# Kernel tuning notes

Measured on AMD Instinct MI355X. Metric: run time of the kernel, lower is better.

The kernel has to match this reference:

```python
import jax, jax.numpy as jnp
import numpy as np

B, S, D, M = 2, 4096, 128, 64

def _linear_init(key, shape, fan_in):
    bound = 1.0 / np.sqrt(fan_in)
    return jax.random.uniform(key, shape, jnp.float32, -bound, bound)

def setup_inputs() -> dict:
    key = jax.random.key(0)
    ks = jax.random.split(key, 18)
    x = jax.random.normal(ks[0], (B, S, D), jnp.float32)
    context = jax.random.normal(ks[1], (B, S, D), jnp.float32)
    # per-mechanism params (torch Linear semantics: y = x @ W.T + b)
    Wt = _linear_init(ks[2], (M, D, D), D)   # transform weight, laid out [m, in, out]
    bt = _linear_init(ks[3], (M, D), D)
    char = jax.random.normal(ks[4], (M, D), jnp.float32)  # characteristics [1,1,d] per mech
    Wg = _linear_init(ks[5], (M, D), D)      # timing_gate weight (out=1)
    bg = _linear_init(ks[6], (M,), D)
    Wv = _linear_init(ks[7], (M, D), D)      # victory_detector weight (out=1)
    bv = _linear_init(ks[8], (M,), D)
    O = jax.random.normal(ks[9], (M, M), jnp.float32) * 0.02  # overcoming matrix
    # selector: Linear(2D,2D) -> GELU -> Linear(2D,M)
    W1 = _linear_init(ks[10], (2 * D, 2 * D), 2 * D)
    b1 = _linear_init(ks[11], (2 * D,), 2 * D)
    W2 = _linear_init(ks[12], (2 * D, M), 2 * D)
    b2 = _linear_init(ks[13], (M,), 2 * D)
    # integrate: Linear(2D, D)
    Wi = _linear_init(ks[14], (2 * D, D), 2 * D)
    bi = _linear_init(ks[15], (D,), 2 * D)
    return {"x": x, "context": context, "Wt": Wt, "bt": bt, "char": char,
            "Wg": Wg, "bg": bg, "Wv": Wv, "bv": bv, "O": O,
            "W1": W1, "b1": b1, "W2": W2, "b2": b2, "Wi": Wi, "bi": bi}

def reference(x, context, Wt, bt, char, Wg, bg, Wv, bv, O, W1, b1, W2, b2, Wi, bi):
    # selection scores over mechanisms
    sel_in = jnp.concatenate([x, context], axis=-1)          # [b,s,2d]
    h = jax.nn.gelu(sel_in @ W1 + b1, approximate=False)
    selection_scores = jax.nn.softmax(h @ W2 + b2, axis=-1)  # [b,s,m]
    # all 64 mechanism nodes as one batched GEMM
    transformed = jnp.einsum('bsd,mde->bsme', x, Wt) + bt + char   # [b,s,m,d]
    timing = jax.nn.sigmoid(jnp.einsum('bsd,md->bsm', x, Wg) + bg)  # [b,s,m]
    victory = jax.nn.sigmoid(jnp.einsum('bsme,me->bsm', transformed, Wv) + bv)
    outputs = transformed * timing[..., None]                # [b,s,m,d]
    # strategic overcoming modulation: gate = 1 + tanh(scores @ O)
    gates = 1.0 + jnp.tanh(selection_scores @ O)             # [b,s,m]
    selected = jnp.einsum('bsme,bsm->bse', outputs, gates * selection_scores)
    victory_potential = jnp.sum(victory * selection_scores, axis=-1)  # [b,s]
    integrated = jnp.concatenate([x, selected], axis=-1) @ Wi + bi    # [b,s,d]
    return integrated, victory_potential
```

## Files before the change

### kernel.cpp

```cpp
#include <hip/hip_runtime.h>
#include <hip/hip_bf16.h>


typedef __bf16 bf16_t;
typedef __bf16 bf16x8 __attribute__((ext_vector_type(8)));
typedef float  f32x4  __attribute__((ext_vector_type(4)));

#define WS_WTT      0u
#define WS_W1T      2097152u
#define WS_W2T      2228224u
#define WS_OT       2260992u
#define WS_WG       2269184u
#define WS_U        2285568u
#define WS_CVEC     2301952u
#define WS_BCT      2302208u
#define WS_WIT      2318592u

#define VP_OFF 1048576

__device__ __forceinline__ f32x4 mfma16(bf16x8 a, bf16x8 b, f32x4 c) {
  return __builtin_amdgcn_mfma_f32_16x16x32_bf16(a, b, c, 0, 0, 0);
}

__device__ __forceinline__ float gelu_exact(float v) {
  return 0.5f * v * (1.0f + erff(v * 0.70710678118654752f));
}
__device__ __forceinline__ float sigmoidf_(float v) {
  return 1.0f / (1.0f + __expf(-v));
}

__device__ __forceinline__ bf16x8 cvt8(float4 v0, float4 v1) {
  bf16x8 a;
  a[0] = (bf16_t)v0.x; a[1] = (bf16_t)v0.y; a[2] = (bf16_t)v0.z; a[3] = (bf16_t)v0.w;
  a[4] = (bf16_t)v1.x; a[5] = (bf16_t)v1.y; a[6] = (bf16_t)v1.z; a[7] = (bf16_t)v1.w;
  return a;
}

__global__ __launch_bounds__(256) void kprep(
    const float* __restrict__ Wt, const float* __restrict__ bt,
    const float* __restrict__ ch, const float* __restrict__ Wg,
    const float* __restrict__ Wv, const float* __restrict__ bv,
    const float* __restrict__ O, const float* __restrict__ W1,
    const float* __restrict__ W2, const float* __restrict__ Wi,
    char* __restrict__ ws)
{
  const int bid = blockIdx.x, tid = threadIdx.x;
  if (bid < 128) {
    const int m = bid >> 1, half = bid & 1;
    const float* wtm = Wt + m * 16384;
    bf16_t* wtt = (bf16_t*)(ws + WS_WTT) + m * 16384;
    const int ks = half * 2 + (tid >> 7), e = tid & 127;
    bf16_t tmp[32];
    #pragma unroll
    for (int dd = 0; dd < 32; ++dd)
      tmp[dd] = (bf16_t)wtm[(ks * 32 + dd) * 128 + e];
    bf16_t* dst = wtt + ks * 4096 + e * 32;
    #pragma unroll
    for (int g = 0; g < 4; ++g)
      *(bf16x8*)(dst + g * 8) = *(const bf16x8*)(tmp + g * 8);
    if (half == 0) {
      if (tid < 128) {
        const float* wvm = Wv + m * 128;
        float s = 0.f;
        for (int e2 = 0; e2 < 128; ++e2) s += wtm[tid * 128 + e2] * wvm[e2];
        ((bf16_t*)(ws + WS_U))[m * 128 + tid] = (bf16_t)s;
      } else if (tid == 128) {
        const float* wvm = Wv + m * 128;
        float s = bv[m];
        for (int e2 = 0; e2 < 128; ++e2) s += (bt[m * 128 + e2] + ch[m * 128 + e2]) * wvm[e2];
        ((float*)(ws + WS_CVEC))[m] = s;
      }
    }
  } else if (bid < 144) {
    int base = (bid - 128) * 256 + tid;
    int k = base >> 4, c0 = (base & 15) * 16;
    bf16_t* o = (bf16_t*)(ws + WS_W1T);
    #pragma unroll
    for (int j = 0; j < 16; ++j) o[(c0 + j) * 256 + k] = (bf16_t)W1[k * 256 + c0 + j];
  } else if (bid < 146) {
    int base = (bid - 144) * 256 + tid;
    int k = base >> 1, c0 = (base & 1) * 32;
    bf16_t* o = (bf16_t*)(ws + WS_W2T);
    #pragma unroll
    for (int j = 0; j < 32; ++j) o[(c0 + j) * 256 + k] = (bf16_t)W2[k * 64 + c0 + j];
  } else if (bid == 146) {
    int k = tid >> 2, c0 = (tid & 3) * 16;
    bf16_t* o = (bf16_t*)(ws + WS_OT);
    #pragma unroll
    for (int j = 0; j < 16; ++j) o[(c0 + j) * 64 + k] = (bf16_t)O[k * 64 + c0 + j];
  } else if (bid == 147) {
    bf16_t* o = (bf16_t*)(ws + WS_WG);
    #pragma unroll
    for (int j = 0; j < 32; ++j) o[tid * 32 + j] = (bf16_t)Wg[tid * 32 + j];
  } else if (bid == 148) {
    bf16_t* o = (bf16_t*)(ws + WS_BCT);
    #pragma unroll
    for (int i = 0; i < 4; ++i) {
      int task = tid + i * 256;
      int m = task >> 4, e0 = (task & 15) * 8;
      #pragma unroll
      for (int j = 0; j < 8; ++j)
        o[(e0 + j) * 64 + m] = (bf16_t)(bt[m * 128 + e0 + j] + ch[m * 128 + e0 + j]);
    }
  } else {
    int base = (bid - 149) * 256 + tid;
    int k = base >> 2, c0 = (base & 3) * 32;
    bf16_t* o = (bf16_t*)(ws + WS_WIT);
    #pragma unroll
    for (int j = 0; j < 32; ++j) o[(c0 + j) * 256 + k] = (bf16_t)Wi[k * 128 + c0 + j];
  }
}

__device__ __forceinline__ void loadF(bf16x8 (&F)[4], const char* bbase, int m) {
  const char* p = bbase + m * 32768;
  F[0] = *(const bf16x8*)(p);
  F[1] = *(const bf16x8*)(p + 8192);
  F[2] = *(const bf16x8*)(p + 16384);
  F[3] = *(const bf16x8*)(p + 24576);
}

template<int J>
__device__ __forceinline__ void computeT(const bf16x8 (&F)[4], const f32x4 (&wc)[16],
                                         const bf16x8 (&aSel)[4][8], f32x4 (&acc)[4]) {
  #pragma unroll
  for (int rg = 0; rg < 4; ++rg) {
    f32x4 y = {0.f, 0.f, 0.f, 0.f};
    #pragma unroll
    for (int ks = 0; ks < 4; ++ks) y = mfma16(aSel[rg][ks], F[ks], y);
    #pragma unroll
    for (int jj = 0; jj < 4; ++jj)
      acc[rg][jj] += wc[rg * 4 + jj][J] * y[jj];
  }
}

__global__ __launch_bounds__(256, 1) void kfused(
    const float* __restrict__ x, const float* __restrict__ ctx,
    const float* __restrict__ b1, const float* __restrict__ b2,
    const float* __restrict__ bg, const float* __restrict__ bi,
    char* __restrict__ ws, float* __restrict__ out)
{
  __shared__ char sm[92160];
  bf16_t* hL      = (bf16_t*)sm;
  float*  scoresL = (float*)(sm + 32768);
  float*  wL      = (float*)(sm + 49152);
  bf16_t* scbL    = (bf16_t*)(sm + 66560);
  bf16_t* wbL     = (bf16_t*)(sm + 74752);
  bf16_t* selL    = (bf16_t*)(sm + 82944);
  float*  vpL     = (float*)(sm + 91136);

  const int tid = threadIdx.x;
  const int lane = tid & 63, wid = tid >> 6;
  const int tb = (blockIdx.x >> 1) * 64;
  const int eh = blockIdx.x & 1;
  const int lr = lane & 15;
  const int lg = lane >> 4;
  const int lk = lg * 8;
  const int lj4 = lg * 4;

  const bf16_t* W1t = (const bf16_t*)(ws + WS_W1T);
  const bf16_t* W2t = (const bf16_t*)(ws + WS_W2T);
  const bf16_t* Ot  = (const bf16_t*)(ws + WS_OT);
  const bf16_t* Wgb = (const bf16_t*)(ws + WS_WG);
  const bf16_t* Ub  = (const bf16_t*)(ws + WS_U);
  const float*  cv  = (const float*)(ws + WS_CVEC);
  const bf16_t* bct = (const bf16_t*)(ws + WS_BCT);
  const bf16_t* Wit = (const bf16_t*)(ws + WS_WIT);
  const char*  wttc = (const char*)(ws + WS_WTT);

  bf16x8 aSel[4][8];
  #pragma unroll
  for (int rg = 0; rg < 4; ++rg) {
    int t = tb + rg * 16 + lr;
    #pragma unroll
    for (int ks = 0; ks < 8; ++ks) {
      const float* src = (ks < 4) ? (x + t * 128 + ks * 32 + lk)
                                  : (ctx + t * 128 + (ks - 4) * 32 + lk);
      aSel[rg][ks] = cvt8(*(const float4*)src, *(const float4*)(src + 4));
    }
  }

  #pragma unroll
  for (int cg = 0; cg < 4; ++cg) {
    int c = wid * 64 + cg * 16 + lr;
    f32x4 a[4] = {{0,0,0,0},{0,0,0,0},{0,0,0,0},{0,0,0,0}};
    #pragma unroll
    for (int ks = 0; ks < 8; ++ks) {
      bf16x8 b = *(const bf16x8*)(W1t + c * 256 + ks * 32 + lk);
      #pragma unroll
      for (int rg = 0; rg < 4; ++rg) a[rg] = mfma16(aSel[rg][ks], b, a[rg]);
    }
    float bb = b1[c];
    #pragma unroll
    for (int rg = 0; rg < 4; ++rg)
      #pragma unroll
      for (int j = 0; j < 4; ++j) {
        int r = rg * 16 + lj4 + j;
        float v = gelu_exact(a[rg][j] + bb);
        *(bf16_t*)((char*)hL + ((r * 512 + c * 2) ^ ((r & 7) << 4))) = (bf16_t)v;
      }
  }
  __syncthreads();

  {
    int c = wid * 16 + lr;
    f32x4 l[4] = {{0,0,0,0},{0,0,0,0},{0,0,0,0},{0,0,0,0}};
    #pragma unroll
    for (int ks = 0; ks < 8; ++ks) {
      int k0 = ks * 32 + lk;
      bf16x8 b = *(const bf16x8*)(W2t + c * 256 + k0);
      #pragma unroll
      for (int rg = 0; rg < 4; ++rg) {
        int r = rg * 16 + lr;
        bf16x8 a = *(const bf16x8*)((char*)hL + ((r * 512 + k0 * 2) ^ ((r & 7) << 4)));
        l[rg] = mfma16(a, b, l[rg]);
      }
    }
    float bb = b2[c];
    #pragma unroll
    for (int rg = 0; rg < 4; ++rg)
      #pragma unroll
      for (int j = 0; j < 4; ++j)
        scoresL[(rg * 16 + lj4 + j) * 64 + c] = l[rg][j] + bb;
  }
  __syncthreads();

  {
    int row = tid >> 2, i = tid & 3;
    float v[16];
    #pragma unroll
    for (int j = 0; j < 16; ++j) v[j] = scoresL[row * 64 + i * 16 + j];
    float mx = v[0];
    #pragma unroll
    for (int j = 1; j < 16; ++j) mx = fmaxf(mx, v[j]);
    mx = fmaxf(mx, __shfl_xor(mx, 1));
    mx = fmaxf(mx, __shfl_xor(mx, 2));
    float sum = 0.f;
    #pragma unroll
    for (int j = 0; j < 16; ++j) { v[j] = __expf(v[j] - mx); sum += v[j]; }
    sum += __shfl_xor(sum, 1);
    sum += __shfl_xor(sum, 2);
    float inv = 1.0f / sum;
    #pragma unroll
    for (int j = 0; j < 16; ++j) {
      float s = v[j] * inv;
      int cc = i * 16 + j;
      scoresL[row * 64 + cc] = s;
      *(bf16_t*)((char*)scbL + ((row * 128 + cc * 2) ^ ((row & 7) << 4))) = (bf16_t)s;
    }
  }
  __syncthreads();

  {
    const int c = wid * 16 + lr;
    f32x4 g[4] = {{0,0,0,0},{0,0,0,0},{0,0,0,0},{0,0,0,0}};
    #pragma unroll
    for (int ks = 0; ks < 2; ++ks) {
      int k0 = ks * 32 + lk;
      bf16x8 b = *(const bf16x8*)(Ot + c * 64 + k0);
      #pragma unroll
      for (int rg = 0; rg < 4; ++rg) {
        int r = rg * 16 + lr;
        bf16x8 a = *(const bf16x8*)((char*)scbL + ((r * 128 + k0 * 2) ^ ((r & 7) << 4)));
        g[rg] = mfma16(a, b, g[rg]);
      }
    }
    f32x4 t[4] = {{0,0,0,0},{0,0,0,0},{0,0,0,0},{0,0,0,0}};
    f32x4 v[4] = {{0,0,0,0},{0,0,0,0},{0,0,0,0},{0,0,0,0}};
    #pragma unroll
    for (int ks = 0; ks < 4; ++ks) {
      bf16x8 bT = *(const bf16x8*)(Wgb + c * 128 + ks * 32 + lk);
      bf16x8 bV = *(const bf16x8*)(Ub  + c * 128 + ks * 32 + lk);
      #pragma unroll
      for (int rg = 0; rg < 4; ++rg) {
        t[rg] = mfma16(aSel[rg][ks], bT, t[rg]);
        v[rg] = mfma16(aSel[rg][ks], bV, v[rg]);
      }
    }
    float bgc = bg[c], cvc = cv[c];
    #pragma unroll
    for (int rg = 0; rg < 4; ++rg)
      #pragma unroll
      for (int j = 0; j < 4; ++j) {
        int r = rg * 16 + lj4 + j;
        float gate = 1.0f + tanhf(g[rg][j]);
        float tim  = sigmoidf_(t[rg][j] + bgc);
        float vic  = sigmoidf_(v[rg][j] + cvc);
        float sc   = scoresL[r * 64 + c];
        float w    = gate * sc * tim;
        wL[r * 68 + c] = w;
        *(bf16_t*)((char*)wbL + ((r * 128 + c * 2) ^ ((r & 7) << 4))) = (bf16_t)w;
        float pv = vic * sc;
        pv += __shfl_xor(pv, 1); pv += __shfl_xor(pv, 2);
        pv += __shfl_xor(pv, 4); pv += __shfl_xor(pv, 8);
        if (lr == 0) vpL[r * 4 + wid] = pv;
      }
  }
  __syncthreads();

  if (eh == 0 && tid < 64) {
    float s = vpL[tid * 4 + 0] + vpL[tid * 4 + 1] + vpL[tid * 4 + 2] + vpL[tid * 4 + 3];
    out[VP_OFF + tb + tid] = s;
  }

  const int wcol = wid * 16;
  f32x4 acc[4] = {{0,0,0,0},{0,0,0,0},{0,0,0,0},{0,0,0,0}};
  {
    int eg = eh * 64 + wcol + lr;
    #pragma unroll
    for (int ks = 0; ks < 2; ++ks) {
      int k0 = ks * 32 + lk;
      bf16x8 b = *(const bf16x8*)(bct + eg * 64 + k0);
      #pragma unroll
      for (int rg = 0; rg < 4; ++rg) {
        int r = rg * 16 + lr;
        bf16x8 a = *(const bf16x8*)((char*)wbL + ((r * 128 + k0 * 2) ^ ((r & 7) << 4)));
        acc[rg] = mfma16(a, b, acc[rg]);
      }
    }
  }

  const char* bbase = wttc + (size_t)(((eh * 64 + wcol + lr) * 32 + lg * 8) * 2);
  bf16x8 F0[4], F1[4], F2[4], F3[4];
  loadF(F0, bbase, 0);
  loadF(F1, bbase, 1);
  loadF(F2, bbase, 2);

  for (int it = 0; it < 16; ++it) {
    const int base = it * 4;
    f32x4 wc[16];
    #pragma unroll
    for (int rg = 0; rg < 4; ++rg)
      #pragma unroll
      for (int jj = 0; jj < 4; ++jj)
        wc[rg * 4 + jj] = *(const f32x4*)(&wL[(rg * 16 + lj4 + jj) * 68 + base]);
    int n4 = base + 4 > 63 ? 63 : base + 4;
    int n5 = base + 5 > 63 ? 63 : base + 5;
    int n6 = base + 6 > 63 ? 63 : base + 6;
    loadF(F3, bbase, base + 3);
    computeT<0>(F0, wc, aSel, acc);
    loadF(F0, bbase, n4);
    computeT<1>(F1, wc, aSel, acc);
    loadF(F1, bbase, n5);
    computeT<2>(F2, wc, aSel, acc);
    loadF(F2, bbase, n6);
    computeT<3>(F3, wc, aSel, acc);
  }

  #pragma unroll
  for (int rg = 0; rg < 4; ++rg)
    #pragma unroll
    for (int j = 0; j < 4; ++j) {
      int r = rg * 16 + lj4 + j;
      int cl = wcol + lr;
      *(bf16_t*)((char*)selL + ((r * 128 + cl * 2) ^ ((r & 7) << 4))) = (bf16_t)acc[rg][j];
    }
  __syncthreads();

  #pragma unroll
  for (int cg = 0; cg < 2; ++cg) {
    int c = wid * 32 + cg * 16 + lr;
    f32x4 a[4] = {{0,0,0,0},{0,0,0,0},{0,0,0,0},{0,0,0,0}};
    #pragma unroll
    for (int ks = 0; ks < 2; ++ks) {
      int k0 = ks * 32 + lk;
      bf16x8 b = *(const bf16x8*)(Wit + c * 256 + 128 + eh * 64 + k0);
      #pragma unroll
      for (int rg = 0; rg < 4; ++rg) {
        int r = rg * 16 + lr;
        bf16x8 av = *(const bf16x8*)((char*)selL + ((r * 128 + k0 * 2) ^ ((r & 7) << 4)));
        a[rg] = mfma16(av, b, a[rg]);
      }
    }
    if (eh == 0) {
      #pragma unroll
      for (int ks = 0; ks < 4; ++ks) {
        bf16x8 b = *(const bf16x8*)(Wit + c * 256 + ks * 32 + lk);
        #pragma unroll
        for (int rg = 0; rg < 4; ++rg) a[rg] = mfma16(aSel[rg][ks], b, a[rg]);
      }
    }
    float bb = (eh == 0) ? bi[c] : 0.0f;
    #pragma unroll
    for (int rg = 0; rg < 4; ++rg)
      #pragma unroll
      for (int j = 0; j < 4; ++j)
        atomicAdd(&out[(tb + rg * 16 + lj4 + j) * 128 + c], a[rg][j] + bb);
  }
}

extern "C" void kernel_launch(void* const* d_in, const int* in_sizes, int n_in,
                              void* d_out, int out_size, void* d_ws, size_t ws_size,
                              hipStream_t stream)
{
  (void)in_sizes; (void)n_in; (void)ws_size;
  const float* x   = (const float*)d_in[0];
  const float* ctx = (const float*)d_in[1];
  const float* Wt  = (const float*)d_in[2];
  const float* bt  = (const float*)d_in[3];
  const float* ch  = (const float*)d_in[4];
  const float* Wg  = (const float*)d_in[5];
  const float* bg  = (const float*)d_in[6];
  const float* Wv  = (const float*)d_in[7];
  const float* bv  = (const float*)d_in[8];
  const float* O   = (const float*)d_in[9];
  const float* W1  = (const float*)d_in[10];
  const float* b1  = (const float*)d_in[11];
  const float* W2  = (const float*)d_in[12];
  const float* b2  = (const float*)d_in[13];
  const float* Wi  = (const float*)d_in[14];
  const float* bi  = (const float*)d_in[15];
  float* out = (float*)d_out;
  char* ws = (char*)d_ws;

  hipMemsetAsync(d_out, 0, (size_t)out_size * 4, stream);
  kprep<<<153, 256, 0, stream>>>(Wt, bt, ch, Wg, Wv, bv, O, W1, W2, Wi, ws);
  kfused<<<256, 256, 0, stream>>>(x, ctx, b1, b2, bg, bi, ws, out);
}
```

Before: 146.8 us.

## Split fused kernel rows across 8 waves and parallelize U/cvec prep

The fused kernel now runs 512 threads per block. Waves are split into two row halves of 32 tokens each, which halves the per-wave register fragments and accumulators and doubles the waves available to hide latency. The softmax pass is remapped to 8 threads per row. In the prep kernel, the serial Wt·Wv reduction and the bias/char·Wv reduction move into dedicated extra blocks that use vectorized float4 loads instead of a long scalar loop in a few blocks. The trade-off is that each wave reloads the Wt B-fragments for fewer rows, which raises L2 and global traffic per useful MFMA.

```diff
diff --git a/kernel.cpp b/kernel.cpp
--- a/kernel.cpp
+++ b/kernel.cpp
@@ -58,19 +58,6 @@
     #pragma unroll
     for (int g = 0; g < 4; ++g)
       *(bf16x8*)(dst + g * 8) = *(const bf16x8*)(tmp + g * 8);
-    if (half == 0) {
-      if (tid < 128) {
-        const float* wvm = Wv + m * 128;
-        float s = 0.f;
-        for (int e2 = 0; e2 < 128; ++e2) s += wtm[tid * 128 + e2] * wvm[e2];
-        ((bf16_t*)(ws + WS_U))[m * 128 + tid] = (bf16_t)s;
-      } else if (tid == 128) {
-        const float* wvm = Wv + m * 128;
-        float s = bv[m];
-        for (int e2 = 0; e2 < 128; ++e2) s += (bt[m * 128 + e2] + ch[m * 128 + e2]) * wvm[e2];
-        ((float*)(ws + WS_CVEC))[m] = s;
-      }
-    }
   } else if (bid < 144) {
     int base = (bid - 128) * 256 + tid;
     int k = base >> 4, c0 = (base & 15) * 16;
@@ -102,12 +89,38 @@
       for (int j = 0; j < 8; ++j)
         o[(e0 + j) * 64 + m] = (bf16_t)(bt[m * 128 + e0 + j] + ch[m * 128 + e0 + j]);
     }
-  } else {
+  } else if (bid < 153) {
     int base = (bid - 149) * 256 + tid;
     int k = base >> 2, c0 = (base & 3) * 32;
     bf16_t* o = (bf16_t*)(ws + WS_WIT);
     #pragma unroll
     for (int j = 0; j < 32; ++j) o[(c0 + j) * 256 + k] = (bf16_t)Wi[k * 128 + c0 + j];
+  } else if (bid < 185) {
+    int task = (bid - 153) * 256 + tid;
+    int m = task >> 7, d = task & 127;
+    const float4* wp = (const float4*)(Wt + m * 16384 + d * 128);
+    const float4* vp = (const float4*)(Wv + m * 128);
+    float s = 0.f;
+    #pragma unroll
+    for (int i = 0; i < 32; ++i) {
+      float4 a = wp[i], b = vp[i];
+      s += a.x * b.x + a.y * b.y + a.z * b.z + a.w * b.w;
+    }
+    ((bf16_t*)(ws + WS_U))[m * 128 + d] = (bf16_t)s;
+  } else {
+    if (tid < 64) {
+      int m = tid;
+      const float4* bp = (const float4*)(bt + m * 128);
+      const float4* cp = (const float4*)(ch + m * 128);
+      const float4* vp = (const float4*)(Wv + m * 128);
+      float s = bv[m];
+      #pragma unroll
+      for (int i = 0; i < 32; ++i) {
+        float4 a = bp[i], c = cp[i], b = vp[i];
+        s += (a.x + c.x) * b.x + (a.y + c.y) * b.y + (a.z + c.z) * b.z + (a.w + c.w) * b.w;
+      }
+      ((float*)(ws + WS_CVEC))[m] = s;
+    }
   }
 }
 
@@ -120,20 +133,20 @@
 }
 
 template<int J>
-__device__ __forceinline__ void computeT(const bf16x8 (&F)[4], const f32x4 (&wc)[16],
-                                         const bf16x8 (&aSel)[4][8], f32x4 (&acc)[4]) {
+__device__ __forceinline__ void computeT(const bf16x8 (&F)[4], const f32x4 (&wc)[8],
+                                         const bf16x8 (&aX)[2][4], f32x4 (&acc)[2]) {
   #pragma unroll
-  for (int rg = 0; rg < 4; ++rg) {
+  for (int rg = 0; rg < 2; ++rg) {
     f32x4 y = {0.f, 0.f, 0.f, 0.f};
     #pragma unroll
-    for (int ks = 0; ks < 4; ++ks) y = mfma16(aSel[rg][ks], F[ks], y);
+    for (int ks = 0; ks < 4; ++ks) y = mfma16(aX[rg][ks], F[ks], y);
     #pragma unroll
     for (int jj = 0; jj < 4; ++jj)
       acc[rg][jj] += wc[rg * 4 + jj][J] * y[jj];
   }
 }
 
-__global__ __launch_bounds__(256, 1) void kfused(
+__global__ __launch_bounds__(512, 2) void kfused(
     const float* __restrict__ x, const float* __restrict__ ctx,
     const float* __restrict__ b1, const float* __restrict__ b2,
     const float* __restrict__ bg, const float* __restrict__ bi,
@@ -150,12 +163,15 @@
 
   const int tid = threadIdx.x;
   const int lane = tid & 63, wid = tid >> 6;
+  const int rh = wid >> 2;
+  const int wq = wid & 3;
   const int tb = (blockIdx.x >> 1) * 64;
   const int eh = blockIdx.x & 1;
   const int lr = lane & 15;
   const int lg = lane >> 4;
   const int lk = lg * 8;
   const int lj4 = lg * 4;
+  const int wr = rh * 32;
 
   const bf16_t* W1t = (const bf16_t*)(ws + WS_W1T);
   const bf16_t* W2t = (const bf16_t*)(ws + WS_W2T);
@@ -167,83 +183,99 @@
   const bf16_t* Wit = (const bf16_t*)(ws + WS_WIT);
   const char*  wttc = (const char*)(ws + WS_WTT);
 
-  bf16x8 aSel[4][8];
+  bf16x8 aX[2][4];
   #pragma unroll
-  for (int rg = 0; rg < 4; ++rg) {
-    int t = tb + rg * 16 + lr;
+  for (int rg = 0; rg < 2; ++rg) {
+    const float* xr = x + (tb + wr + rg * 16 + lr) * 128;
+    #pragma unroll
+    for (int ks = 0; ks < 4; ++ks)
+      aX[rg][ks] = cvt8(*(const float4*)(xr + ks * 32 + lk),
+                        *(const float4*)(xr + ks * 32 + lk + 4));
+  }
+
+  {
+    f32x4 a1[4][2] = {{{0,0,0,0},{0,0,0,0}},{{0,0,0,0},{0,0,0,0}},
+                      {{0,0,0,0},{0,0,0,0}},{{0,0,0,0},{0,0,0,0}}};
     #pragma unroll
     for (int ks = 0; ks < 8; ++ks) {
-      const float* src = (ks < 4) ? (x + t * 128 + ks * 32 + lk)
-                                  : (ctx + t * 128 + (ks - 4) * 32 + lk);
-      aSel[rg][ks] = cvt8(*(const float4*)src, *(const float4*)(src + 4));
-    }
-  }
-
-  #pragma unroll
-  for (int cg = 0; cg < 4; ++cg) {
-    int c = wid * 64 + cg * 16 + lr;
-    f32x4 a[4] = {{0,0,0,0},{0,0,0,0},{0,0,0,0},{0,0,0,0}};
-    #pragma unroll
-    for (int ks = 0; ks < 8; ++ks) {
-      bf16x8 b = *(const bf16x8*)(W1t + c * 256 + ks * 32 + lk);
-      #pragma unroll
-      for (int rg = 0; rg < 4; ++rg) a[rg] = mfma16(aSel[rg][ks], b, a[rg]);
-    }
-    float bb = b1[c];
-    #pragma unroll
-    for (int rg = 0; rg < 4; ++rg)
-      #pragma unroll
-      for (int j = 0; j < 4; ++j) {
-        int r = rg * 16 + lj4 + j;
-        float v = gelu_exact(a[rg][j] + bb);
-        *(bf16_t*)((char*)hL + ((r * 512 + c * 2) ^ ((r & 7) << 4))) = (bf16_t)v;
-      }
+      bf16x8 af[2];
+      if (ks < 4) {
+        af[0] = aX[0][ks]; af[1] = aX[1][ks];
+      } else {
+        #pragma unroll
+        for (int rg = 0; rg < 2; ++rg) {
+          const float* cr = ctx + (tb + wr + rg * 16 + lr) * 128 + (ks - 4) * 32 + lk;
+          af[rg] = cvt8(*(const float4*)cr, *(const float4*)(cr + 4));
+        }
+      }
+      #pragma unroll
+      for (int cg = 0; cg < 4; ++cg) {
+        bf16x8 b = *(const bf16x8*)(W1t + (wq * 64 + cg * 16 + lr) * 256 + ks * 32 + lk);
+        a1[cg][0] = mfma16(af[0], b, a1[cg][0]);
+        a1[cg][1] = mfma16(af[1], b, a1[cg][1]);
+      }
+    }
+    #pragma unroll
+    for (int cg = 0; cg < 4; ++cg) {
+      int c = wq * 64 + cg * 16 + lr;
+      float bb = b1[c];
+      #pragma unroll
+      for (int rg = 0; rg < 2; ++rg)
+        #pragma unroll
+        for (int j = 0; j < 4; ++j) {
+          int r = wr + rg * 16 + lj4 + j;
+          float v = gelu_exact(a1[cg][rg][j] + bb);
+          *(bf16_t*)((char*)hL + ((r * 512 + c * 2) ^ ((r & 7) << 4))) = (bf16_t)v;
+        }
+    }
   }
   __syncthreads();
 
   {
-    int c = wid * 16 + lr;
-    f32x4 l[4] = {{0,0,0,0},{0,0,0,0},{0,0,0,0},{0,0,0,0}};
+    int c = wq * 16 + lr;
+    f32x4 l[2] = {{0,0,0,0},{0,0,0,0}};
     #pragma unroll
     for (int ks = 0; ks < 8; ++ks) {
       int k0 = ks * 32 + lk;
       bf16x8 b = *(const bf16x8*)(W2t + c * 256 + k0);
       #pragma unroll
-      for (int rg = 0; rg < 4; ++rg) {
-        int r = rg * 16 + lr;
+      for (int rg = 0; rg < 2; ++rg) {
+        int r = wr + rg * 16 + lr;
         bf16x8 a = *(const bf16x8*)((char*)hL + ((r * 512 + k0 * 2) ^ ((r & 7) << 4)));
         l[rg] = mfma16(a, b, l[rg]);
       }
     }
     float bb = b2[c];
     #pragma unroll
-    for (int rg = 0; rg < 4; ++rg)
+    for (int rg = 0; rg < 2; ++rg)
       #pragma unroll
       for (int j = 0; j < 4; ++j)
-        scoresL[(rg * 16 + lj4 + j) * 64 + c] = l[rg][j] + bb;
+        scoresL[(wr + rg * 16 + lj4 + j) * 64 + c] = l[rg][j] + bb;
   }
   __syncthreads();
 
   {
-    int row = tid >> 2, i = tid & 3;
-    float v[16];
-    #pragma unroll
-    for (int j = 0; j < 16; ++j) v[j] = scoresL[row * 64 + i * 16 + j];
+    int row = tid >> 3, i = tid & 7;
+    float v[8];
+    #pragma unroll
+    for (int j = 0; j < 8; ++j) v[j] = scoresL[row * 64 + i * 8 + j];
     float mx = v[0];
     #pragma unroll
-    for (int j = 1; j < 16; ++j) mx = fmaxf(mx, v[j]);
+    for (int j = 1; j < 8; ++j) mx = fmaxf(mx, v[j]);
     mx = fmaxf(mx, __shfl_xor(mx, 1));
     mx = fmaxf(mx, __shfl_xor(mx, 2));
+    mx = fmaxf(mx, __shfl_xor(mx, 4));
     float sum = 0.f;
     #pragma unroll
-    for (int j = 0; j < 16; ++j) { v[j] = __expf(v[j] - mx); sum += v[j]; }
+    for (int j = 0; j < 8; ++j) { v[j] = __expf(v[j] - mx); sum += v[j]; }
     sum += __shfl_xor(sum, 1);
     sum += __shfl_xor(sum, 2);
+    sum += __shfl_xor(sum, 4);
     float inv = 1.0f / sum;
     #pragma unroll
-    for (int j = 0; j < 16; ++j) {
+    for (int j = 0; j < 8; ++j) {
       float s = v[j] * inv;
-      int cc = i * 16 + j;
+      int cc = i * 8 + j;
       scoresL[row * 64 + cc] = s;
       *(bf16_t*)((char*)scbL + ((row * 128 + cc * 2) ^ ((row & 7) << 4))) = (bf16_t)s;
     }
@@ -251,37 +283,37 @@
   __syncthreads();
 
   {
-    const int c = wid * 16 + lr;
-    f32x4 g[4] = {{0,0,0,0},{0,0,0,0},{0,0,0,0},{0,0,0,0}};
+    const int c = wq * 16 + lr;
+    f32x4 g[2] = {{0,0,0,0},{0,0,0,0}};
     #pragma unroll
     for (int ks = 0; ks < 2; ++ks) {
       int k0 = ks * 32 + lk;
       bf16x8 b = *(const bf16x8*)(Ot + c * 64 + k0);
       #pragma unroll
-      for (int rg = 0; rg < 4; ++rg) {
-        int r = rg * 16 + lr;
+      for (int rg = 0; rg < 2; ++rg) {
+        int r = wr + rg * 16 + lr;
         bf16x8 a = *(const bf16x8*)((char*)scbL + ((r * 128 + k0 * 2) ^ ((r & 7) << 4)));
         g[rg] = mfma16(a, b, g[rg]);
       }
     }
-    f32x4 t[4] = {{0,0,0,0},{0,0,0,0},{0,0,0,0},{0,0,0,0}};
-    f32x4 v[4] = {{0,0,0,0},{0,0,0,0},{0,0,0,0},{0,0,0,0}};
+    f32x4 t[2] = {{0,0,0,0},{0,0,0,0}};
+    f32x4 v[2] = {{0,0,0,0},{0,0,0,0}};
     #pragma unroll
     for (int ks = 0; ks < 4; ++ks) {
       bf16x8 bT = *(const bf16x8*)(Wgb + c * 128 + ks * 32 + lk);
       bf16x8 bV = *(const bf16x8*)(Ub  + c * 128 + ks * 32 + lk);
       #pragma unroll
-      for (int rg = 0; rg < 4; ++rg) {
-        t[rg] = mfma16(aSel[rg][ks], bT, t[rg]);
-        v[rg] = mfma16(aSel[rg][ks], bV, v[rg]);
+      for (int rg = 0; rg < 2; ++rg) {
+        t[rg] = mfma16(aX[rg][ks], bT, t[rg]);
+        v[rg] = mfma16(aX[rg][ks], bV, v[rg]);
       }
     }
     float bgc = bg[c], cvc = cv[c];
     #pragma unroll
-    for (int rg = 0; rg < 4; ++rg)
+    for (int rg = 0; rg < 2; ++rg)
       #pragma unroll
       for (int j = 0; j < 4; ++j) {
-        int r = rg * 16 + lj4 + j;
+        int r = wr + rg * 16 + lj4 + j;
         float gate = 1.0f + tanhf(g[rg][j]);
         float tim  = sigmoidf_(t[rg][j] + bgc);
         float vic  = sigmoidf_(v[rg][j] + cvc);
@@ -292,7 +324,7 @@
         float pv = vic * sc;
         pv += __shfl_xor(pv, 1); pv += __shfl_xor(pv, 2);
         pv += __shfl_xor(pv, 4); pv += __shfl_xor(pv, 8);
-        if (lr == 0) vpL[r * 4 + wid] = pv;
+        if (lr == 0) vpL[r * 4 + wq] = pv;
       }
   }
   __syncthreads();
@@ -302,24 +334,23 @@
     out[VP_OFF + tb + tid] = s;
   }
 
-  const int wcol = wid * 16;
-  f32x4 acc[4] = {{0,0,0,0},{0,0,0,0},{0,0,0,0},{0,0,0,0}};
+  f32x4 acc[2] = {{0,0,0,0},{0,0,0,0}};
   {
-    int eg = eh * 64 + wcol + lr;
+    int eg = eh * 64 + wq * 16 + lr;
     #pragma unroll
     for (int ks = 0; ks < 2; ++ks) {
       int k0 = ks * 32 + lk;
       bf16x8 b = *(const bf16x8*)(bct + eg * 64 + k0);
       #pragma unroll
-      for (int rg = 0; rg < 4; ++rg) {
-        int r = rg * 16 + lr;
+      for (int rg = 0; rg < 2; ++rg) {
+        int r = wr + rg * 16 + lr;
         bf16x8 a = *(const bf16x8*)((char*)wbL + ((r * 128 + k0 * 2) ^ ((r & 7) << 4)));
         acc[rg] = mfma16(a, b, acc[rg]);
       }
     }
   }
 
-  const char* bbase = wttc + (size_t)(((eh * 64 + wcol + lr) * 32 + lg * 8) * 2);
+  const char* bbase = wttc + (size_t)(((eh * 64 + wq * 16 + lr) * 32 + lg * 8) * 2);
   bf16x8 F0[4], F1[4], F2[4], F3[4];
   loadF(F0, bbase, 0);
   loadF(F1, bbase, 1);
@@ -327,46 +358,46 @@
 
   for (int it = 0; it < 16; ++it) {
     const int base = it * 4;
-    f32x4 wc[16];
-    #pragma unroll
-    for (int rg = 0; rg < 4; ++rg)
+    f32x4 wc[8];
+    #pragma unroll
+    for (int rg = 0; rg < 2; ++rg)
       #pragma unroll
       for (int jj = 0; jj < 4; ++jj)
-        wc[rg * 4 + jj] = *(const f32x4*)(&wL[(rg * 16 + lj4 + jj) * 68 + base]);
+        wc[rg * 4 + jj] = *(const f32x4*)(&wL[(wr + rg * 16 + lj4 + jj) * 68 + base]);
     int n4 = base + 4 > 63 ? 63 : base + 4;
     int n5 = base + 5 > 63 ? 63 : base + 5;
     int n6 = base + 6 > 63 ? 63 : base + 6;
     loadF(F3, bbase, base + 3);
-    computeT<0>(F0, wc, aSel, acc);
+    computeT<0>(F0, wc, aX, acc);
     loadF(F0, bbase, n4);
-    computeT<1>(F1, wc, aSel, acc);
+    computeT<1>(F1, wc, aX, acc);
     loadF(F1, bbase, n5);
-    computeT<2>(F2, wc, aSel, acc);
+    computeT<2>(F2, wc, aX, acc);
     loadF(F2, bbase, n6);
-    computeT<3>(F3, wc, aSel, acc);
+    computeT<3>(F3, wc, aX, acc);
   }
 
   #pragma unroll
-  for (int rg = 0; rg < 4; ++rg)
+  for (int rg = 0; rg < 2; ++rg)
     #pragma unroll
     for (int j = 0; j < 4; ++j) {
-      int r = rg * 16 + lj4 + j;
-      int cl = wcol + lr;
+      int r = wr + rg * 16 + lj4 + j;
+      int cl = wq * 16 + lr;
       *(bf16_t*)((char*)selL + ((r * 128 + cl * 2) ^ ((r & 7) << 4))) = (bf16_t)acc[rg][j];
     }
   __syncthreads();
 
   #pragma unroll
   for (int cg = 0; cg < 2; ++cg) {
-    int c = wid * 32 + cg * 16 + lr;
-    f32x4 a[4] = {{0,0,0,0},{0,0,0,0},{0,0,0,0},{0,0,0,0}};
+    int c = wq * 32 + cg * 16 + lr;
+    f32x4 a[2] = {{0,0,0,0},{0,0,0,0}};
     #pragma unroll
     for (int ks = 0; ks < 2; ++ks) {
       int k0 = ks * 32 + lk;
       bf16x8 b = *(const bf16x8*)(Wit + c * 256 + 128 + eh * 64 + k0);
       #pragma unroll
-      for (int rg = 0; rg < 4; ++rg) {
-        int r = rg * 16 + lr;
+      for (int rg = 0; rg < 2; ++rg) {
+        int r = wr + rg * 16 + lr;
         bf16x8 av = *(const bf16x8*)((char*)selL + ((r * 128 + k0 * 2) ^ ((r & 7) << 4)));
         a[rg] = mfma16(av, b, a[rg]);
       }
@@ -376,15 +407,15 @@
       for (int ks = 0; ks < 4; ++ks) {
         bf16x8 b = *(const bf16x8*)(Wit + c * 256 + ks * 32 + lk);
         #pragma unroll
-        for (int rg = 0; rg < 4; ++rg) a[rg] = mfma16(aSel[rg][ks], b, a[rg]);
+        for (int rg = 0; rg < 2; ++rg) a[rg] = mfma16(aX[rg][ks], b, a[rg]);
       }
     }
     float bb = (eh == 0) ? bi[c] : 0.0f;
     #pragma unroll
-    for (int rg = 0; rg < 4; ++rg)
+    for (int rg = 0; rg < 2; ++rg)
       #pragma unroll
       for (int j = 0; j < 4; ++j)
-        atomicAdd(&out[(tb + rg * 16 + lj4 + j) * 128 + c], a[rg][j] + bb);
+        atomicAdd(&out[(tb + wr + rg * 16 + lj4 + j) * 128 + c], a[rg][j] + bb);
   }
 }
 
@@ -413,6 +444,6 @@
   char* ws = (char*)d_ws;
 
   hipMemsetAsync(d_out, 0, (size_t)out_size * 4, stream);
-  kprep<<<153, 256, 0, stream>>>(Wt, bt, ch, Wg, Wv, bv, O, W1, W2, Wi, ws);
-  kfused<<<256, 256, 0, stream>>>(x, ctx, b1, b2, bg, bi, ws, out);
-}
+  kprep<<<186, 256, 0, stream>>>(Wt, bt, ch, Wg, Wv, bv, O, W1, W2, Wi, ws);
+  kfused<<<256, 512, 0, stream>>>(x, ctx, b1, b2, bg, bi, ws, out);
+}
```

After: 159.8 us. 1.09x slower.
